# Optimization experiments

Hardware: AMD Instinct MI355X
Metric: run time of the kernel (lower is better)

Reference implementation:

```python
import jax, jax.numpy as jnp
import numpy as np

N = 20000      # nodes
E = 320000     # edges
G = 64         # graphs in batch
PD = 9         # property input dim (properties='yyyyyyyyy')
KD = 32        # kernel_dim (node feature dim)
MD = 32        # m_dim (message dim)
FF = 32        # fourier_features
NK = 5         # n_kernels
EIN = FF * 2 + KD + 1 + KD * 2  # 161, edge MLP input dim
MLP = 256
EPS = 1e-5


def layer_norm(x, g, b):
    mu = jnp.mean(x, -1, keepdims=True)
    var = jnp.mean((x - mu) ** 2, -1, keepdims=True)
    return (x - mu) * jax.lax.rsqrt(var + EPS) * g + b


def silu(x):
    return x * jax.nn.sigmoid(x)


def setup_inputs() -> dict:
    key = jax.random.key(0)
    ks = jax.random.split(key, 20)
    rn = lambda k, s: jax.random.normal(k, s, dtype=jnp.float32) * 0.1
    inp = {}
    inp["props"] = jax.random.normal(ks[0], (N, PD), dtype=jnp.float32)
    inp["positions"] = jax.random.normal(ks[1], (N, 3), dtype=jnp.float32)
    inp["edge_props"] = jax.random.normal(ks[2], (E, PD), dtype=jnp.float32)
    inp["embed_W"] = rn(ks[3], (PD, KD)); inp["embed_b"] = jnp.zeros((KD,), jnp.float32)
    inp["edge_embed_W"] = rn(ks[4], (PD, KD)); inp["edge_embed_b"] = jnp.zeros((KD,), jnp.float32)
    # per-kernel params stacked over NK
    inp["k_eW1"] = rn(ks[5], (NK, EIN, EIN * 2)); inp["k_eb1"] = jnp.zeros((NK, EIN * 2), jnp.float32)
    inp["k_eW2"] = rn(ks[6], (NK, EIN * 2, MD)); inp["k_eb2"] = jnp.zeros((NK, MD), jnp.float32)
    inp["k_eln_g"] = jnp.ones((NK, MD), jnp.float32); inp["k_eln_b"] = jnp.zeros((NK, MD), jnp.float32)
    inp["k_nln1_g"] = jnp.ones((NK, KD), jnp.float32); inp["k_nln1_b"] = jnp.zeros((NK, KD), jnp.float32)
    inp["k_nln2_g"] = jnp.ones((NK, KD), jnp.float32); inp["k_nln2_b"] = jnp.zeros((NK, KD), jnp.float32)
    inp["k_nW1"] = rn(ks[7], (NK, KD + MD, KD * 2)); inp["k_nb1"] = jnp.zeros((NK, KD * 2), jnp.float32)
    inp["k_nW2"] = rn(ks[8], (NK, KD * 2, KD)); inp["k_nb2"] = jnp.zeros((NK, KD), jnp.float32)
    inp["fnn_W0"] = rn(ks[9], (KD * (NK + 1), MLP)); inp["fnn_b0"] = jnp.zeros((MLP,), jnp.float32)
    inp["fnn_W1"] = rn(ks[10], (MLP, MLP)); inp["fnn_b1"] = jnp.zeros((MLP,), jnp.float32)
    inp["fnn_W2"] = rn(ks[11], (MLP, MLP)); inp["fnn_b2"] = jnp.zeros((MLP,), jnp.float32)
    inp["fnn_W3"] = rn(ks[12], (MLP, 1)); inp["fnn_b3"] = jnp.zeros((1,), jnp.float32)
    inp["edge_index"] = jax.random.randint(ks[13], (2, E), 0, N, dtype=jnp.int64)
    inp["batch"] = jnp.sort(jax.random.randint(ks[14], (N,), 0, G, dtype=jnp.int64))
    return inp


def egnn_forward(props, positions, edge_props, embed_W, embed_b, edge_embed_W, edge_embed_b,
                 k_eW1, k_eb1, k_eW2, k_eb2, k_eln_g, k_eln_b, k_nln1_g, k_nln1_b,
                 k_nln2_g, k_nln2_b, k_nW1, k_nb1, k_nW2, k_nb2,
                 fnn_W0, fnn_b0, fnn_W1, fnn_b1, fnn_W2, fnn_b2, fnn_W3, fnn_b3,
                 edge_index, batch):
    src, dst = edge_index[0], edge_index[1]  # x_j = source, x_i = target (PyG)
    feats = props @ embed_W + embed_b                     # EmbedNCP (properties-only path)
    edge_feats = edge_props @ edge_embed_W + edge_embed_b  # EmbedEdge
    coords = positions
    # coords are never updated, so the distance/fourier features are the same each round
    rel_coords = coords[src] - coords[dst]
    rel_dist = jnp.sum(rel_coords ** 2, -1, keepdims=True)  # [E,1] squared distance
    scales = 2.0 ** jnp.arange(FF, dtype=jnp.float32)
    d = rel_dist / scales                                    # [E,FF]
    fdist = jnp.concatenate([jnp.sin(d), jnp.cos(d), rel_dist], -1)  # [E,2FF+1]
    edge_attr = jnp.concatenate([fdist, edge_feats], -1)     # [E, 2FF+1+KD]
    deg = jax.ops.segment_sum(jnp.ones((E,), feats.dtype), dst, num_segments=N)
    deg = jnp.maximum(deg, 1.0)[:, None]
    feat_list = [feats]
    for k in range(NK):
        h = jnp.concatenate([feats[dst], feats[src], edge_attr], -1)  # [E, EIN]
        h = silu(h @ k_eW1[k] + k_eb1[k])
        m_ij = silu(h @ k_eW2[k] + k_eb2[k])
        m_ij = layer_norm(m_ij, k_eln_g[k], k_eln_b[k])               # edge_norm1
        m_i = jax.ops.segment_sum(m_ij, dst, num_segments=N) / deg    # mean aggregate
        m_i = layer_norm(m_i, k_eln_g[k], k_eln_b[k])                 # edge_norm1 again (as in source)
        hf = layer_norm(feats, k_nln1_g[k], k_nln1_b[k])
        h2 = jnp.concatenate([hf, m_i], -1)
        h2 = silu(h2 @ k_nW1[k] + k_nb1[k])
        h2 = h2 @ k_nW2[k] + k_nb2[k]
        h2 = layer_norm(h2, k_nln2_g[k], k_nln2_b[k])
        feats = feats + h2                                            # residual
        feat_list.append(feats)
    allf = jnp.concatenate(feat_list, -1)                             # [N, KD*(NK+1)]
    gsum = jax.ops.segment_sum(allf, batch, num_segments=G)
    gcnt = jnp.maximum(jax.ops.segment_sum(jnp.ones((N,), allf.dtype), batch, num_segments=G), 1.0)[:, None]
    g = gsum / gcnt                                                   # mean pool per graph
    g = silu(g @ fnn_W0 + fnn_b0)
    g = silu(g @ fnn_W1 + fnn_b1)
    g = silu(g @ fnn_W2 + fnn_b2)
    return g @ fnn_W3 + fnn_b3                                        # [G, 1]


def reference(props, positions, edge_props, embed_W, embed_b, edge_embed_W, edge_embed_b,
              k_eW1, k_eb1, k_eW2, k_eb2, k_eln_g, k_eln_b, k_nln1_g, k_nln1_b,
              k_nln2_g, k_nln2_b, k_nW1, k_nb1, k_nW2, k_nb2,
              fnn_W0, fnn_b0, fnn_W1, fnn_b1, fnn_W2, fnn_b2, fnn_W3, fnn_b3,
              edge_index, batch):
    return egnn_forward(props, positions, edge_props, embed_W, embed_b, edge_embed_W, edge_embed_b,
                        k_eW1, k_eb1, k_eW2, k_eb2, k_eln_g, k_eln_b, k_nln1_g, k_nln1_b,
                        k_nln2_g, k_nln2_b, k_nW1, k_nb1, k_nW2, k_nb2,
                        fnn_W0, fnn_b0, fnn_W1, fnn_b1, fnn_W2, fnn_b2, fnn_W3, fnn_b3,
                        edge_index, batch)
```

## Files before the change

kernel.cpp:

```cpp
#include <hip/hip_runtime.h>
#include <math.h>

#define N_NODES 20000
#define N_EDGES 320000
#define N_GRAPHS 64
#define PD 9
#define KD 32
#define MD 32
#define NK 5
#define EIN 161
#define EIN2 322
#define ALLF (KD*(NK+1))
#define LN_EPS 1e-5f

typedef __attribute__((ext_vector_type(8))) short short8;
typedef __attribute__((ext_vector_type(4))) float f32x4;
typedef __attribute__((ext_vector_type(4))) unsigned u32x4;
typedef __attribute__((ext_vector_type(2))) unsigned u32x2;
typedef __attribute__((ext_vector_type(4))) int i32x4;

__device__ __forceinline__ float silu_f(float x) { return x / (1.f + __expf(-x)); }

__device__ __forceinline__ unsigned short f2bf(float x) {
    union { float f; unsigned u; } v; v.f = x;
    unsigned r = v.u + 0x7FFFu + ((v.u >> 16) & 1u);
    return (unsigned short)(r >> 16);
}

__device__ __forceinline__ unsigned cvt_pk_bf16(float lo, float hi) {
    unsigned r;
    asm("v_cvt_pk_bf16_f32 %0, %1, %2" : "=v"(r) : "v"(lo), "v"(hi));
    return r;
}

__global__ __launch_bounds__(256) void pack_w1_kernel(
    const float* __restrict__ eW1, unsigned short* __restrict__ W1p)
{
    int fid = blockIdx.x * 256 + threadIdx.x;
    if (fid >= NK*21*5*64) return;
    int kk = fid / (21*5*64);
    int r  = fid % (21*5*64);
    int nt = r / (5*64);
    int r2 = r % (5*64);
    int kb = r2 >> 6;
    int l  = r2 & 63;
    int q = l >> 4, el = l & 15;
    int n = 32*(nt >> 1) + 8*(el >> 2) + 4*(nt & 1) + (el & 3);
    short8 out;
    #pragma unroll
    for (int i = 0; i < 8; ++i) {
        int kp = 32*kb + 8*q + i;
        int orig = (kp < 128) ? kp : kp + 1;
        float v = (n < EIN2) ? eW1[((size_t)kk*EIN + orig)*EIN2 + n] : 0.f;
        out[i] = (short)f2bf(v);
    }
    *(short8*)&W1p[(size_t)fid*8] = out;
}

__global__ __launch_bounds__(256) void pack_w2_kernel(
    const float* __restrict__ eW2, unsigned short* __restrict__ W2p)
{
    int fid = blockIdx.x * 256 + threadIdx.x;
    if (fid >= NK*2*11*64) return;
    int kk = fid / (2*11*64);
    int r  = fid % (2*11*64);
    int nt2 = r / (11*64);
    int r2  = r % (11*64);
    int kb2 = r2 >> 6;
    int l   = r2 & 63;
    int q = l >> 4, el = l & 15;
    int n = 16*nt2 + el;
    short8 out;
    #pragma unroll
    for (int i = 0; i < 8; ++i) {
        int k2 = 32*kb2 + 8*q + i;
        float v = (k2 < EIN2) ? eW2[((size_t)kk*EIN2 + k2)*MD + n] : 0.f;
        out[i] = (short)f2bf(v);
    }
    *(short8*)&W2p[(size_t)fid*8] = out;
}

__global__ __launch_bounds__(256) void pack_nw_kernel(
    const float* __restrict__ nW1, const float* __restrict__ nW2,
    unsigned short* __restrict__ W1A, unsigned short* __restrict__ W2A)
{
    int fid = blockIdx.x * 256 + threadIdx.x;
    const int tot1 = NK*4*2*64;
    const int tot2 = NK*2*2*64;
    if (fid < tot1) {
        int kk = fid / (4*2*64);
        int r  = fid % (4*2*64);
        int mt = r / 128;
        int r2 = r % 128;
        int kb = r2 >> 6;
        int l  = r2 & 63;
        int q = l >> 4, el = l & 15;
        int n = 32*(mt >> 1) + 8*(el >> 2) + 4*(mt & 1) + (el & 3);
        short8 out;
        #pragma unroll
        for (int i = 0; i < 8; ++i)
            out[i] = (short)f2bf(nW1[((size_t)kk*64 + 32*kb + 8*q + i)*64 + n]);
        *(short8*)&W1A[(size_t)fid*8] = out;
    } else if (fid < tot1 + tot2) {
        int f2 = fid - tot1;
        int kk = f2 / (2*2*64);
        int r  = f2 % (2*2*64);
        int mt2 = r / 128;
        int r2  = r % 128;
        int kb  = r2 >> 6;
        int l   = r2 & 63;
        int q = l >> 4, el = l & 15;
        short8 out;
        #pragma unroll
        for (int i = 0; i < 8; ++i)
            out[i] = (short)f2bf(nW2[((size_t)kk*64 + 32*kb + 8*q + i)*32 + 16*mt2 + el]);
        *(short8*)&W2A[(size_t)f2*8] = out;
    }
}

__global__ __launch_bounds__(256) void embed_nodes_kernel(
    const float* __restrict__ props, const float* __restrict__ W,
    const float* __restrict__ b,
    float* __restrict__ feats, unsigned short* __restrict__ feats_bf,
    float* __restrict__ allf)
{
    int t = threadIdx.x;
    int n = blockIdx.x * 8 + (t >> 5);
    int f = t & 31;
    if (n >= N_NODES) return;
    float acc = b[f];
    #pragma unroll
    for (int i = 0; i < PD; ++i) acc += props[n*PD + i] * W[i*KD + f];
    feats[n*KD + f] = acc;
    feats_bf[n*KD + f] = f2bf(acc);
    allf[(size_t)n*ALLF + f] = acc;
}

__global__ __launch_bounds__(256) void edge_prep_kernel(
    const float* __restrict__ edge_props, const float* __restrict__ positions,
    const int* __restrict__ ei, const float* __restrict__ W,
    const float* __restrict__ b, float* __restrict__ rel,
    float* __restrict__ deg, unsigned short* __restrict__ constpack)
{
    __shared__ float ef[64*32];
    __shared__ float rdl[64];
    int t = threadIdx.x;
    int b0 = blockIdx.x;
    int e0 = b0 * 64;

    {
        int e = t >> 2, sub = t & 3;
        float acc[8];
        #pragma unroll
        for (int j = 0; j < 8; ++j) acc[j] = b[sub*8 + j];
        #pragma unroll
        for (int i = 0; i < PD; ++i) {
            float p = edge_props[(size_t)(e0 + e)*PD + i];
            #pragma unroll
            for (int j = 0; j < 8; ++j) acc[j] += p * W[i*KD + sub*8 + j];
        }
        #pragma unroll
        for (int j = 0; j < 8; ++j) ef[e*32 + sub*8 + j] = acc[j];
    }
    if (t < 64) {
        int e = e0 + t;
        int s = ei[e], d = ei[N_EDGES + e];
        float dx = positions[s*3+0] - positions[d*3+0];
        float dy = positions[s*3+1] - positions[d*3+1];
        float dz = positions[s*3+2] - positions[d*3+2];
        float rd = dx*dx + dy*dy + dz*dz;
        rdl[t] = rd;
        rel[e] = rd;
        atomicAdd(&deg[d], 1.f);
    }
    __syncthreads();

    int l = t & 63, w = t >> 6;
    int q = l >> 4, el = l & 15;
    float rd = rdl[16*w + el];
    #pragma unroll
    for (int kbr = 0; kbr < 3; ++kbr) {
        short8 out;
        #pragma unroll
        for (int i = 0; i < 8; ++i) {
            int k = 8*q + i;
            float v;
            if (kbr == 0)      v = sinf(ldexpf(rd, -k));
            else if (kbr == 1) v = cosf(ldexpf(rd, -k));
            else               v = ef[(16*w + el)*32 + k];
            out[i] = (short)f2bf(v);
        }
        *(short8*)&constpack[((((size_t)b0*4 + w)*3 + kbr)*64 + l)*8] = out;
    }
}

__global__ __launch_bounds__(256) void edge_mlp_mfma(
    const unsigned short* __restrict__ feats_bf,
    const unsigned short* __restrict__ constpack,
    const float* __restrict__ rel, const int* __restrict__ ei,
    const unsigned short* __restrict__ W1p, const unsigned short* __restrict__ W2p,
    const float* __restrict__ w1rd, const float* __restrict__ eb1,
    const float* __restrict__ eb2, const float* __restrict__ lg,
    const float* __restrict__ lb, float* __restrict__ msum)
{
    int t = threadIdx.x;
    int b = blockIdx.x;
    int w = t >> 6, l = t & 63, q = l >> 4, el = l & 15;
    int e0 = b * 64;
    int eMine = e0 + 16*w + el;
    int srcn = ei[eMine];
    int dstn = ei[N_EDGES + eMine];
    float rd = rel[eMine];

    short8 a0 = *(const short8*)&feats_bf[(size_t)dstn*KD + 8*q];
    short8 a1 = *(const short8*)&feats_bf[(size_t)srcn*KD + 8*q];
    const unsigned short* cp = &constpack[((size_t)(b*4 + w)*3)*512 + (size_t)l*8];
    short8 a2 = *(const short8*)&cp[0];
    short8 a3 = *(const short8*)&cp[512];
    short8 a4 = *(const short8*)&cp[1024];

    f32x4 acc20 = {0.f, 0.f, 0.f, 0.f};
    f32x4 acc21 = {0.f, 0.f, 0.f, 0.f};
    unsigned pk0 = 0u, pk1 = 0u, pk2 = 0u, pk3 = 0u;

    #pragma unroll
    for (int nt = 0; nt < 21; ++nt) {
        f32x4 aA = {0.f, 0.f, 0.f, 0.f};
        f32x4 aB = {0.f, 0.f, 0.f, 0.f};
        const unsigned short* wb = &W1p[(size_t)(nt*5)*512 + (size_t)l*8];
        aA = __builtin_amdgcn_mfma_f32_16x16x32_bf16(*(const short8*)&wb[0],    a0, aA, 0, 0, 0);
        aA = __builtin_amdgcn_mfma_f32_16x16x32_bf16(*(const short8*)&wb[512],  a1, aA, 0, 0, 0);
        aA = __builtin_amdgcn_mfma_f32_16x16x32_bf16(*(const short8*)&wb[1024], a2, aA, 0, 0, 0);
        aB = __builtin_amdgcn_mfma_f32_16x16x32_bf16(*(const short8*)&wb[1536], a3, aB, 0, 0, 0);
        aB = __builtin_amdgcn_mfma_f32_16x16x32_bf16(*(const short8*)&wb[2048], a4, aB, 0, 0, 0);

        int base = 32*(nt >> 1) + 4*(nt & 1) + 8*q;
        float vj[4];
        if (nt < 20) {
            f32x4 be = *(const f32x4*)&eb1[base];
            f32x4 wr = *(const f32x4*)&w1rd[base];
            #pragma unroll
            for (int j = 0; j < 4; ++j)
                vj[j] = silu_f(aA[j] + aB[j] + be[j] + rd * wr[j]);
        } else {
            #pragma unroll
            for (int j = 0; j < 4; ++j) {
                int n1 = base + j;
                bool ok = n1 < EIN2;
                float be = ok ? eb1[n1] : 0.f;
                float wr = ok ? w1rd[n1] : 0.f;
                float v = silu_f(aA[j] + aB[j] + be + rd * wr);
                vj[j] = ok ? v : 0.f;
            }
        }

        if ((nt & 1) == 0) {
            pk0 = cvt_pk_bf16(vj[0], vj[1]);
            pk1 = cvt_pk_bf16(vj[2], vj[3]);
        } else {
            pk2 = cvt_pk_bf16(vj[0], vj[1]);
            pk3 = cvt_pk_bf16(vj[2], vj[3]);
            const int kb2 = nt >> 1;
            u32x4 hv = { pk0, pk1, pk2, pk3 };
            short8 av = __builtin_bit_cast(short8, hv);
            short8 b0 = *(const short8*)&W2p[(size_t)kb2*512 + (size_t)l*8];
            short8 b1 = *(const short8*)&W2p[(size_t)(11 + kb2)*512 + (size_t)l*8];
            acc20 = __builtin_amdgcn_mfma_f32_16x16x32_bf16(av, b0, acc20, 0, 0, 0);
            acc21 = __builtin_amdgcn_mfma_f32_16x16x32_bf16(av, b1, acc21, 0, 0, 0);
        }
    }
    {
        u32x4 hv = { pk0, pk1, 0u, 0u };
        short8 av = __builtin_bit_cast(short8, hv);
        short8 b0 = *(const short8*)&W2p[(size_t)10*512 + (size_t)l*8];
        short8 b1 = *(const short8*)&W2p[(size_t)21*512 + (size_t)l*8];
        acc20 = __builtin_amdgcn_mfma_f32_16x16x32_bf16(av, b0, acc20, 0, 0, 0);
        acc21 = __builtin_amdgcn_mfma_f32_16x16x32_bf16(av, b1, acc21, 0, 0, 0);
    }

    i32x4 dstv = *(const i32x4*)&ei[N_EDGES + e0 + 16*w + 4*q];
    float e20 = eb2[el], e21 = eb2[16 + el];
    float g0v = lg[el],  g1v = lg[16 + el];
    float b0v = lb[el],  b1v = lb[16 + el];
    #pragma unroll
    for (int j = 0; j < 4; ++j) {
        float m0 = silu_f(acc20[j] + e20);
        float m1 = silu_f(acc21[j] + e21);
        float s = m0 + m1;
        s += __shfl_xor(s, 1, 16); s += __shfl_xor(s, 2, 16);
        s += __shfl_xor(s, 4, 16); s += __shfl_xor(s, 8, 16);
        float mu = s * (1.f/32.f);
        float d0 = m0 - mu, d1 = m1 - mu;
        float vv = d0*d0 + d1*d1;
        vv += __shfl_xor(vv, 1, 16); vv += __shfl_xor(vv, 2, 16);
        vv += __shfl_xor(vv, 4, 16); vv += __shfl_xor(vv, 8, 16);
        float rs = rsqrtf(vv * (1.f/32.f) + LN_EPS);
        int dst = dstv[j];
        atomicAdd(&msum[(size_t)dst*MD + el],      d0*rs*g0v + b0v);
        atomicAdd(&msum[(size_t)dst*MD + 16 + el], d1*rs*g1v + b1v);
    }
}

__global__ __launch_bounds__(256) void node_mlp_mfma(
    const float* __restrict__ msum, const float* __restrict__ deg,
    const unsigned short* __restrict__ W1A, const unsigned short* __restrict__ W2A,
    const float* __restrict__ nb1, const float* __restrict__ nb2,
    const float* __restrict__ eln_g, const float* __restrict__ eln_b,
    const float* __restrict__ n1g, const float* __restrict__ n1b,
    const float* __restrict__ n2g, const float* __restrict__ n2b,
    float* __restrict__ feats, unsigned short* __restrict__ feats_bf,
    float* __restrict__ allf, int kslot)
{
    int t = threadIdx.x;
    int w = t >> 6, l = t & 63, q = l >> 4, el = l & 15;
    int nd = blockIdx.x*64 + 16*w + el;
    bool okn = nd < N_NODES;
    size_t ndc = okn ? (size_t)nd : (size_t)(N_NODES - 1);

    float x[2][8];
    {
        f32x4 f0 = *(const f32x4*)&feats[ndc*KD + 8*q];
        f32x4 f1 = *(const f32x4*)&feats[ndc*KD + 8*q + 4];
        float inv = 1.f / fmaxf(deg[ndc], 1.f);
        f32x4 m0 = *(const f32x4*)&msum[ndc*KD + 8*q];
        f32x4 m1 = *(const f32x4*)&msum[ndc*KD + 8*q + 4];
        #pragma unroll
        for (int j = 0; j < 4; ++j) {
            x[0][j] = f0[j]; x[0][4+j] = f1[j];
            x[1][j] = m0[j]*inv; x[1][4+j] = m1[j]*inv;
        }
    }
    short8 xf[2];
    #pragma unroll
    for (int kb = 0; kb < 2; ++kb) {
        float s = 0.f;
        #pragma unroll
        for (int i = 0; i < 8; ++i) s += x[kb][i];
        s += __shfl_xor(s, 16); s += __shfl_xor(s, 32);
        float mu = s * (1.f/32.f);
        float vv = 0.f;
        #pragma unroll
        for (int i = 0; i < 8; ++i) { float d = x[kb][i] - mu; vv += d*d; }
        vv += __shfl_xor(vv, 16); vv += __shfl_xor(vv, 32);
        float rs = rsqrtf(vv * (1.f/32.f) + LN_EPS);
        const float* gp = kb ? eln_g : n1g;
        const float* bp = kb ? eln_b : n1b;
        f32x4 ga = *(const f32x4*)&gp[8*q];
        f32x4 gb = *(const f32x4*)&gp[8*q + 4];
        f32x4 ba = *(const f32x4*)&bp[8*q];
        f32x4 bb = *(const f32x4*)&bp[8*q + 4];
        float z[8];
        #pragma unroll
        for (int j = 0; j < 4; ++j) {
            z[j]   = (x[kb][j]   - mu)*rs*ga[j] + ba[j];
            z[4+j] = (x[kb][4+j] - mu)*rs*gb[j] + bb[j];
        }
        u32x4 pv = { cvt_pk_bf16(z[0], z[1]), cvt_pk_bf16(z[2], z[3]),
                     cvt_pk_bf16(z[4], z[5]), cvt_pk_bf16(z[6], z[7]) };
        xf[kb] = __builtin_bit_cast(short8, pv);
    }

    unsigned hr[8];
    #pragma unroll
    for (int mt = 0; mt < 4; ++mt) {
        f32x4 acc = {0.f, 0.f, 0.f, 0.f};
        acc = __builtin_amdgcn_mfma_f32_16x16x32_bf16(
            *(const short8*)&W1A[(size_t)(mt*2 + 0)*512 + (size_t)l*8], xf[0], acc, 0, 0, 0);
        acc = __builtin_amdgcn_mfma_f32_16x16x32_bf16(
            *(const short8*)&W1A[(size_t)(mt*2 + 1)*512 + (size_t)l*8], xf[1], acc, 0, 0, 0);
        int base = 32*(mt >> 1) + 4*(mt & 1) + 8*q;
        f32x4 b1v = *(const f32x4*)&nb1[base];
        float vj[4];
        #pragma unroll
        for (int j = 0; j < 4; ++j) vj[j] = silu_f(acc[j] + b1v[j]);
        int ix = (mt >> 1)*4 + (mt & 1)*2;
        hr[ix]     = cvt_pk_bf16(vj[0], vj[1]);
        hr[ix + 1] = cvt_pk_bf16(vj[2], vj[3]);
    }

    u32x4 h0v = { hr[0], hr[1], hr[2], hr[3] };
    u32x4 h1v = { hr[4], hr[5], hr[6], hr[7] };
    short8 hf0 = __builtin_bit_cast(short8, h0v);
    short8 hf1 = __builtin_bit_cast(short8, h1v);
    float o[2][4];
    #pragma unroll
    for (int mt2 = 0; mt2 < 2; ++mt2) {
        f32x4 acc = {0.f, 0.f, 0.f, 0.f};
        acc = __builtin_amdgcn_mfma_f32_16x16x32_bf16(
            *(const short8*)&W2A[(size_t)(mt2*2 + 0)*512 + (size_t)l*8], hf0, acc, 0, 0, 0);
        acc = __builtin_amdgcn_mfma_f32_16x16x32_bf16(
            *(const short8*)&W2A[(size_t)(mt2*2 + 1)*512 + (size_t)l*8], hf1, acc, 0, 0, 0);
        f32x4 b2v = *(const f32x4*)&nb2[16*mt2 + 4*q];
        #pragma unroll
        for (int j = 0; j < 4; ++j) o[mt2][j] = acc[j] + b2v[j];
    }
    float s2 = 0.f;
    #pragma unroll
    for (int mt2 = 0; mt2 < 2; ++mt2)
        #pragma unroll
        for (int j = 0; j < 4; ++j) s2 += o[mt2][j];
    s2 += __shfl_xor(s2, 16); s2 += __shfl_xor(s2, 32);
    float mu2 = s2 * (1.f/32.f);
    float vv2 = 0.f;
    #pragma unroll
    for (int mt2 = 0; mt2 < 2; ++mt2)
        #pragma unroll
        for (int j = 0; j < 4; ++j) { float d = o[mt2][j] - mu2; vv2 += d*d; }
    vv2 += __shfl_xor(vv2, 16); vv2 += __shfl_xor(vv2, 32);
    float rs2 = rsqrtf(vv2 * (1.f/32.f) + LN_EPS);

    #pragma unroll
    for (int mt2 = 0; mt2 < 2; ++mt2) {
        f32x4 gv = *(const f32x4*)&n2g[16*mt2 + 4*q];
        f32x4 bv = *(const f32x4*)&n2b[16*mt2 + 4*q];
        f32x4 fold = *(const f32x4*)&feats[ndc*KD + 16*mt2 + 4*q];
        f32x4 nf;
        #pragma unroll
        for (int j = 0; j < 4; ++j)
            nf[j] = fold[j] + (o[mt2][j] - mu2)*rs2*gv[j] + bv[j];
        if (okn) {
            *(f32x4*)&feats[(size_t)nd*KD + 16*mt2 + 4*q] = nf;
            u32x2 pb = { cvt_pk_bf16(nf[0], nf[1]), cvt_pk_bf16(nf[2], nf[3]) };
            *(u32x2*)&feats_bf[(size_t)nd*KD + 16*mt2 + 4*q] = pb;
            *(f32x4*)&allf[(size_t)nd*ALLF + kslot*KD + 16*mt2 + 4*q] = nf;
        }
    }
}

__global__ __launch_bounds__(256) void pool_kernel(
    const float* __restrict__ allf, const int* __restrict__ batch,
    float* __restrict__ gsum, float* __restrict__ gcnt)
{
    int b = blockIdx.x, t = threadIdx.x;
    int g = b >> 2, part = b & 3;
    int lo = 0, hi = N_NODES;
    while (lo < hi) { int m = (lo+hi) >> 1; if (batch[m] < g) lo = m+1; else hi = m; }
    int start = lo;
    hi = N_NODES;
    while (lo < hi) { int m = (lo+hi) >> 1; if (batch[m] < g+1) lo = m+1; else hi = m; }
    int end = lo;
    if (part == 0 && t == 0) gcnt[g] = (float)(end - start);
    int len = end - start;
    int chunk = (len + 3) >> 2;
    int s = start + part*chunk;
    int e = min(end, s + chunk);
    if (t < ALLF && e > s) {
        float acc = 0.f;
        for (int n = s; n < e; ++n) acc += allf[(size_t)n*ALLF + t];
        atomicAdd(&gsum[g*ALLF + t], acc);
    }
}

__global__ __launch_bounds__(256) void fnn_kernel(
    const float* __restrict__ gsum, const float* __restrict__ gcnt,
    const float* __restrict__ W0, const float* __restrict__ b0,
    const float* __restrict__ W1, const float* __restrict__ b1,
    const float* __restrict__ W2, const float* __restrict__ b2,
    const float* __restrict__ W3, const float* __restrict__ b3,
    float* __restrict__ out)
{
    __shared__ float xs[256];
    __shared__ float partial[4];
    int g = blockIdx.x, t = threadIdx.x;
    float inv = 1.f / fmaxf(gcnt[g], 1.f);
    if (t < ALLF) xs[t] = gsum[g*ALLF + t] * inv;
    __syncthreads();
    float acc = b0[t];
    for (int i = 0; i < ALLF; ++i) acc += xs[i] * W0[i*256 + t];
    acc = silu_f(acc);
    __syncthreads(); xs[t] = acc; __syncthreads();
    acc = b1[t];
    for (int i = 0; i < 256; ++i) acc += xs[i] * W1[i*256 + t];
    acc = silu_f(acc);
    __syncthreads(); xs[t] = acc; __syncthreads();
    acc = b2[t];
    for (int i = 0; i < 256; ++i) acc += xs[i] * W2[i*256 + t];
    acc = silu_f(acc);
    __syncthreads(); xs[t] = acc; __syncthreads();
    float v = xs[t] * W3[t];
    #pragma unroll
    for (int m = 32; m; m >>= 1) v += __shfl_xor(v, m, 64);
    if ((t & 63) == 0) partial[t >> 6] = v;
    __syncthreads();
    if (t == 0) out[g] = partial[0] + partial[1] + partial[2] + partial[3] + b3[0];
}

extern "C" void kernel_launch(void* const* d_in, const int* in_sizes, int n_in,
                              void* d_out, int out_size, void* d_ws, size_t ws_size,
                              hipStream_t stream) {
    const float* props      = (const float*)d_in[0];
    const float* positions  = (const float*)d_in[1];
    const float* edge_props = (const float*)d_in[2];
    const float* embed_W    = (const float*)d_in[3];
    const float* embed_b    = (const float*)d_in[4];
    const float* eeW        = (const float*)d_in[5];
    const float* eeb        = (const float*)d_in[6];
    const float* k_eW1      = (const float*)d_in[7];
    const float* k_eb1      = (const float*)d_in[8];
    const float* k_eW2      = (const float*)d_in[9];
    const float* k_eb2      = (const float*)d_in[10];
    const float* k_eln_g    = (const float*)d_in[11];
    const float* k_eln_b    = (const float*)d_in[12];
    const float* k_n1g      = (const float*)d_in[13];
    const float* k_n1b      = (const float*)d_in[14];
    const float* k_n2g      = (const float*)d_in[15];
    const float* k_n2b      = (const float*)d_in[16];
    const float* k_nW1      = (const float*)d_in[17];
    const float* k_nb1      = (const float*)d_in[18];
    const float* k_nW2      = (const float*)d_in[19];
    const float* k_nb2      = (const float*)d_in[20];
    const float* fnn_W0     = (const float*)d_in[21];
    const float* fnn_b0     = (const float*)d_in[22];
    const float* fnn_W1     = (const float*)d_in[23];
    const float* fnn_b1     = (const float*)d_in[24];
    const float* fnn_W2     = (const float*)d_in[25];
    const float* fnn_b2     = (const float*)d_in[26];
    const float* fnn_W3     = (const float*)d_in[27];
    const float* fnn_b3     = (const float*)d_in[28];
    const int*   ei         = (const int*)d_in[29];
    const int*   batch      = (const int*)d_in[30];
    float* out = (float*)d_out;

    char* wsb = (char*)d_ws;
    size_t off = 0;
    #define WS_ALLOC(ptr_t, name, bytes) ptr_t name = (ptr_t)(wsb + off); off += (((size_t)(bytes)) + 255) & ~(size_t)255;
    WS_ALLOC(float*, feats, (size_t)N_NODES*KD*4)
    WS_ALLOC(float*, msum,  (size_t)N_NODES*KD*4)
    WS_ALLOC(float*, deg,   (size_t)N_NODES*4)
    WS_ALLOC(float*, rel,   (size_t)N_EDGES*4)
    WS_ALLOC(float*, gsum,  (size_t)N_GRAPHS*ALLF*4)
    WS_ALLOC(float*, gcnt,  (size_t)N_GRAPHS*4)
    WS_ALLOC(float*, allf,  (size_t)N_NODES*ALLF*4)
    WS_ALLOC(unsigned short*, feats_bf,  (size_t)N_NODES*KD*2)
    WS_ALLOC(unsigned short*, constpack, (size_t)5000*4*3*64*8*2)
    WS_ALLOC(unsigned short*, W1p,  (size_t)NK*21*5*64*8*2)
    WS_ALLOC(unsigned short*, W2p,  (size_t)NK*2*11*64*8*2)
    WS_ALLOC(unsigned short*, W1An, (size_t)NK*4*2*64*8*2)
    WS_ALLOC(unsigned short*, W2An, (size_t)NK*2*2*64*8*2)
    (void)ws_size;

    hipMemsetAsync(deg,  0, (size_t)N_NODES*4, stream);
    hipMemsetAsync(gsum, 0, (size_t)N_GRAPHS*ALLF*4, stream);

    pack_w1_kernel<<<(NK*21*5*64 + 255)/256, 256, 0, stream>>>(k_eW1, W1p);
    pack_w2_kernel<<<(NK*2*11*64 + 255)/256, 256, 0, stream>>>(k_eW2, W2p);
    pack_nw_kernel<<<(NK*4*2*64 + NK*2*2*64 + 255)/256, 256, 0, stream>>>(k_nW1, k_nW2, W1An, W2An);
    embed_nodes_kernel<<<N_NODES/8, 256, 0, stream>>>(props, embed_W, embed_b,
                                                      feats, feats_bf, allf);
    edge_prep_kernel<<<N_EDGES/64, 256, 0, stream>>>(edge_props, positions, ei, eeW, eeb,
                                                     rel, deg, constpack);

    for (int k = 0; k < NK; ++k) {
        hipMemsetAsync(msum, 0, (size_t)N_NODES*KD*4, stream);
        edge_mlp_mfma<<<N_EDGES/64, 256, 0, stream>>>(
            feats_bf, constpack, rel, ei,
            W1p + (size_t)k*21*5*512, W2p + (size_t)k*2*11*512,
            k_eW1 + (size_t)k*EIN*EIN2 + 128*EIN2,
            k_eb1 + (size_t)k*EIN2, k_eb2 + (size_t)k*MD,
            k_eln_g + (size_t)k*MD, k_eln_b + (size_t)k*MD, msum);
        node_mlp_mfma<<<(N_NODES + 63)/64, 256, 0, stream>>>(
            msum, deg,
            W1An + (size_t)k*4*2*512, W2An + (size_t)k*2*2*512,
            k_nb1 + (size_t)k*64, k_nb2 + (size_t)k*32,
            k_eln_g + (size_t)k*MD, k_eln_b + (size_t)k*MD,
            k_n1g + (size_t)k*KD, k_n1b + (size_t)k*KD,
            k_n2g + (size_t)k*KD, k_n2b + (size_t)k*KD,
            feats, feats_bf, allf, k+1);
    }

    pool_kernel<<<N_GRAPHS*4, 256, 0, stream>>>(allf, batch, gsum, gcnt);
    fnn_kernel<<<N_GRAPHS, 256, 0, stream>>>(gsum, gcnt, fnn_W0, fnn_b0, fnn_W1, fnn_b1,
                                             fnn_W2, fnn_b2, fnn_W3, fnn_b3, out);
}
```

Before: 829.8 us.

## Switch edge MLP to 32x32x16 MFMA tiles with bias folded into weights

The edge MLP moves from 16x16x32 bf16 MFMA to 32x32x16 MFMA, so each wave handles 32 edges and each block 128 edges. The weight and constant packing layouts are rebuilt to match. The first-layer bias and the rel-distance column are folded into the packed W1 as extra K rows, fed by a constant-1/rd operand, which removes the per-element bias and rd FMA epilogue. The aim is to cut weight-load traffic per edge and epilogue ALU work. In exchange the rd term now goes through bf16, and register pressure from the 16-wide accumulators rises.

```diff
diff --git a/kernel.cpp b/kernel.cpp
--- a/kernel.cpp
+++ b/kernel.cpp
@@ -15,9 +15,9 @@
 
 typedef __attribute__((ext_vector_type(8))) short short8;
 typedef __attribute__((ext_vector_type(4))) float f32x4;
+typedef __attribute__((ext_vector_type(16))) float f32x16;
 typedef __attribute__((ext_vector_type(4))) unsigned u32x4;
 typedef __attribute__((ext_vector_type(2))) unsigned u32x2;
-typedef __attribute__((ext_vector_type(4))) int i32x4;
 
 __device__ __forceinline__ float silu_f(float x) { return x / (1.f + __expf(-x)); }
 
@@ -34,24 +34,31 @@
 }
 
 __global__ __launch_bounds__(256) void pack_w1_kernel(
-    const float* __restrict__ eW1, unsigned short* __restrict__ W1p)
+    const float* __restrict__ eW1, const float* __restrict__ eb1,
+    unsigned short* __restrict__ W1p)
 {
     int fid = blockIdx.x * 256 + threadIdx.x;
-    if (fid >= NK*21*5*64) return;
-    int kk = fid / (21*5*64);
-    int r  = fid % (21*5*64);
-    int nt = r / (5*64);
-    int r2 = r % (5*64);
-    int kb = r2 >> 6;
+    if (fid >= NK*11*11*64) return;
+    int kk = fid / (11*11*64);
+    int r  = fid % (11*11*64);
+    int m  = r / (11*64);
+    int r2 = r % (11*64);
+    int s  = r2 >> 6;
     int l  = r2 & 63;
-    int q = l >> 4, el = l & 15;
-    int n = 32*(nt >> 1) + 8*(el >> 2) + 4*(nt & 1) + (el & 3);
+    int p = l & 31, khalf = l >> 5;
+    int h = (p >> 2) & 1, c = p & 3, bb = p >> 3;
+    int n = 32*m + 16*(bb >> 1) + 8*h + c + 4*(bb & 1);
     short8 out;
     #pragma unroll
     for (int i = 0; i < 8; ++i) {
-        int kp = 32*kb + 8*q + i;
-        int orig = (kp < 128) ? kp : kp + 1;
-        float v = (n < EIN2) ? eW1[((size_t)kk*EIN + orig)*EIN2 + n] : 0.f;
+        int k = 16*s + 8*khalf + i;
+        float v = 0.f;
+        if (n < EIN2) {
+            if (k < 128)       v = eW1[((size_t)kk*EIN + k)*EIN2 + n];
+            else if (k < 160)  v = eW1[((size_t)kk*EIN + k + 1)*EIN2 + n];
+            else if (k == 160) v = eb1[(size_t)kk*EIN2 + n];
+            else if (k == 161) v = eW1[((size_t)kk*EIN + 128)*EIN2 + n];
+        }
         out[i] = (short)f2bf(v);
     }
     *(short8*)&W1p[(size_t)fid*8] = out;
@@ -61,19 +68,16 @@
     const float* __restrict__ eW2, unsigned short* __restrict__ W2p)
 {
     int fid = blockIdx.x * 256 + threadIdx.x;
-    if (fid >= NK*2*11*64) return;
-    int kk = fid / (2*11*64);
-    int r  = fid % (2*11*64);
-    int nt2 = r / (11*64);
-    int r2  = r % (11*64);
-    int kb2 = r2 >> 6;
-    int l   = r2 & 63;
-    int q = l >> 4, el = l & 15;
-    int n = 16*nt2 + el;
+    if (fid >= NK*22*64) return;
+    int kk = fid / (22*64);
+    int r  = fid % (22*64);
+    int s2 = r >> 6;
+    int l  = r & 63;
+    int n = l & 31, khalf = l >> 5;
     short8 out;
     #pragma unroll
     for (int i = 0; i < 8; ++i) {
-        int k2 = 32*kb2 + 8*q + i;
+        int k2 = 16*s2 + 8*khalf + i;
         float v = (k2 < EIN2) ? eW2[((size_t)kk*EIN2 + k2)*MD + n] : 0.f;
         out[i] = (short)f2bf(v);
     }
@@ -142,27 +146,27 @@
     const float* __restrict__ b, float* __restrict__ rel,
     float* __restrict__ deg, unsigned short* __restrict__ constpack)
 {
-    __shared__ float ef[64*32];
-    __shared__ float rdl[64];
+    __shared__ float ef[128*32];
+    __shared__ float rdl[128];
     int t = threadIdx.x;
     int b0 = blockIdx.x;
-    int e0 = b0 * 64;
+    int e0 = b0 * 128;
 
     {
-        int e = t >> 2, sub = t & 3;
-        float acc[8];
-        #pragma unroll
-        for (int j = 0; j < 8; ++j) acc[j] = b[sub*8 + j];
+        int e = t >> 1, sub = t & 1;
+        float acc[16];
+        #pragma unroll
+        for (int j = 0; j < 16; ++j) acc[j] = b[sub*16 + j];
         #pragma unroll
         for (int i = 0; i < PD; ++i) {
             float p = edge_props[(size_t)(e0 + e)*PD + i];
             #pragma unroll
-            for (int j = 0; j < 8; ++j) acc[j] += p * W[i*KD + sub*8 + j];
-        }
-        #pragma unroll
-        for (int j = 0; j < 8; ++j) ef[e*32 + sub*8 + j] = acc[j];
-    }
-    if (t < 64) {
+            for (int j = 0; j < 16; ++j) acc[j] += p * W[i*KD + sub*16 + j];
+        }
+        #pragma unroll
+        for (int j = 0; j < 16; ++j) ef[e*32 + sub*16 + j] = acc[j];
+    }
+    if (t < 128) {
         int e = e0 + t;
         int s = ei[e], d = ei[N_EDGES + e];
         float dx = positions[s*3+0] - positions[d*3+0];
@@ -176,21 +180,23 @@
     __syncthreads();
 
     int l = t & 63, w = t >> 6;
-    int q = l >> 4, el = l & 15;
-    float rd = rdl[16*w + el];
-    #pragma unroll
-    for (int kbr = 0; kbr < 3; ++kbr) {
+    int e32 = l & 31, hi = l >> 5;
+    int eloc = 32*w + e32;
+    float rd = rdl[eloc];
+    #pragma unroll
+    for (int slot = 0; slot < 6; ++slot) {
+        int grp = slot >> 1, half = slot & 1;
         short8 out;
         #pragma unroll
         for (int i = 0; i < 8; ++i) {
-            int k = 8*q + i;
+            int off = 16*half + 8*hi + i;
             float v;
-            if (kbr == 0)      v = sinf(ldexpf(rd, -k));
-            else if (kbr == 1) v = cosf(ldexpf(rd, -k));
-            else               v = ef[(16*w + el)*32 + k];
+            if (grp == 0)      v = sinf(ldexpf(rd, -off));
+            else if (grp == 1) v = cosf(ldexpf(rd, -off));
+            else               v = ef[eloc*32 + off];
             out[i] = (short)f2bf(v);
         }
-        *(short8*)&constpack[((((size_t)b0*4 + w)*3 + kbr)*64 + l)*8] = out;
+        *(short8*)&constpack[(((size_t)b0*4 + w)*6 + slot)*512 + (size_t)l*8] = out;
     }
 }
 
@@ -199,105 +205,88 @@
     const unsigned short* __restrict__ constpack,
     const float* __restrict__ rel, const int* __restrict__ ei,
     const unsigned short* __restrict__ W1p, const unsigned short* __restrict__ W2p,
-    const float* __restrict__ w1rd, const float* __restrict__ eb1,
     const float* __restrict__ eb2, const float* __restrict__ lg,
     const float* __restrict__ lb, float* __restrict__ msum)
 {
     int t = threadIdx.x;
     int b = blockIdx.x;
-    int w = t >> 6, l = t & 63, q = l >> 4, el = l & 15;
-    int e0 = b * 64;
-    int eMine = e0 + 16*w + el;
-    int srcn = ei[eMine];
-    int dstn = ei[N_EDGES + eMine];
-    float rd = rel[eMine];
-
-    short8 a0 = *(const short8*)&feats_bf[(size_t)dstn*KD + 8*q];
-    short8 a1 = *(const short8*)&feats_bf[(size_t)srcn*KD + 8*q];
-    const unsigned short* cp = &constpack[((size_t)(b*4 + w)*3)*512 + (size_t)l*8];
-    short8 a2 = *(const short8*)&cp[0];
-    short8 a3 = *(const short8*)&cp[512];
-    short8 a4 = *(const short8*)&cp[1024];
-
-    f32x4 acc20 = {0.f, 0.f, 0.f, 0.f};
-    f32x4 acc21 = {0.f, 0.f, 0.f, 0.f};
-    unsigned pk0 = 0u, pk1 = 0u, pk2 = 0u, pk3 = 0u;
-
-    #pragma unroll
-    for (int nt = 0; nt < 21; ++nt) {
-        f32x4 aA = {0.f, 0.f, 0.f, 0.f};
-        f32x4 aB = {0.f, 0.f, 0.f, 0.f};
-        const unsigned short* wb = &W1p[(size_t)(nt*5)*512 + (size_t)l*8];
-        aA = __builtin_amdgcn_mfma_f32_16x16x32_bf16(*(const short8*)&wb[0],    a0, aA, 0, 0, 0);
-        aA = __builtin_amdgcn_mfma_f32_16x16x32_bf16(*(const short8*)&wb[512],  a1, aA, 0, 0, 0);
-        aA = __builtin_amdgcn_mfma_f32_16x16x32_bf16(*(const short8*)&wb[1024], a2, aA, 0, 0, 0);
-        aB = __builtin_amdgcn_mfma_f32_16x16x32_bf16(*(const short8*)&wb[1536], a3, aB, 0, 0, 0);
-        aB = __builtin_amdgcn_mfma_f32_16x16x32_bf16(*(const short8*)&wb[2048], a4, aB, 0, 0, 0);
-
-        int base = 32*(nt >> 1) + 4*(nt & 1) + 8*q;
-        float vj[4];
-        if (nt < 20) {
-            f32x4 be = *(const f32x4*)&eb1[base];
-            f32x4 wr = *(const f32x4*)&w1rd[base];
-            #pragma unroll
-            for (int j = 0; j < 4; ++j)
-                vj[j] = silu_f(aA[j] + aB[j] + be[j] + rd * wr[j]);
-        } else {
-            #pragma unroll
-            for (int j = 0; j < 4; ++j) {
-                int n1 = base + j;
-                bool ok = n1 < EIN2;
-                float be = ok ? eb1[n1] : 0.f;
-                float wr = ok ? w1rd[n1] : 0.f;
-                float v = silu_f(aA[j] + aB[j] + be + rd * wr);
-                vj[j] = ok ? v : 0.f;
-            }
-        }
-
-        if ((nt & 1) == 0) {
-            pk0 = cvt_pk_bf16(vj[0], vj[1]);
-            pk1 = cvt_pk_bf16(vj[2], vj[3]);
-        } else {
-            pk2 = cvt_pk_bf16(vj[0], vj[1]);
-            pk3 = cvt_pk_bf16(vj[2], vj[3]);
-            const int kb2 = nt >> 1;
-            u32x4 hv = { pk0, pk1, pk2, pk3 };
-            short8 av = __builtin_bit_cast(short8, hv);
-            short8 b0 = *(const short8*)&W2p[(size_t)kb2*512 + (size_t)l*8];
-            short8 b1 = *(const short8*)&W2p[(size_t)(11 + kb2)*512 + (size_t)l*8];
-            acc20 = __builtin_amdgcn_mfma_f32_16x16x32_bf16(av, b0, acc20, 0, 0, 0);
-            acc21 = __builtin_amdgcn_mfma_f32_16x16x32_bf16(av, b1, acc21, 0, 0, 0);
-        }
-    }
+    int w = t >> 6, l = t & 63, e32 = l & 31, hi = l >> 5;
+    int edge = b*128 + 32*w + e32;
+    int srcn = ei[edge];
+    int dstn = ei[N_EDGES + edge];
+    float rd = rel[edge];
+
+    short8 bf[11];
+    bf[0] = *(const short8*)&feats_bf[(size_t)dstn*KD + 8*hi];
+    bf[1] = *(const short8*)&feats_bf[(size_t)dstn*KD + 16 + 8*hi];
+    bf[2] = *(const short8*)&feats_bf[(size_t)srcn*KD + 8*hi];
+    bf[3] = *(const short8*)&feats_bf[(size_t)srcn*KD + 16 + 8*hi];
+    const unsigned short* cp = &constpack[(((size_t)b*4 + w)*6)*512 + (size_t)l*8];
+    #pragma unroll
+    for (int slot = 0; slot < 6; ++slot)
+        bf[4 + slot] = *(const short8*)&cp[(size_t)slot*512];
     {
-        u32x4 hv = { pk0, pk1, 0u, 0u };
-        short8 av = __builtin_bit_cast(short8, hv);
-        short8 b0 = *(const short8*)&W2p[(size_t)10*512 + (size_t)l*8];
-        short8 b1 = *(const short8*)&W2p[(size_t)21*512 + (size_t)l*8];
-        acc20 = __builtin_amdgcn_mfma_f32_16x16x32_bf16(av, b0, acc20, 0, 0, 0);
-        acc21 = __builtin_amdgcn_mfma_f32_16x16x32_bf16(av, b1, acc21, 0, 0, 0);
-    }
-
-    i32x4 dstv = *(const i32x4*)&ei[N_EDGES + e0 + 16*w + 4*q];
-    float e20 = eb2[el], e21 = eb2[16 + el];
-    float g0v = lg[el],  g1v = lg[16 + el];
-    float b0v = lb[el],  b1v = lb[16 + el];
-    #pragma unroll
-    for (int j = 0; j < 4; ++j) {
-        float m0 = silu_f(acc20[j] + e20);
-        float m1 = silu_f(acc21[j] + e21);
-        float s = m0 + m1;
-        s += __shfl_xor(s, 1, 16); s += __shfl_xor(s, 2, 16);
-        s += __shfl_xor(s, 4, 16); s += __shfl_xor(s, 8, 16);
-        float mu = s * (1.f/32.f);
-        float d0 = m0 - mu, d1 = m1 - mu;
-        float vv = d0*d0 + d1*d1;
-        vv += __shfl_xor(vv, 1, 16); vv += __shfl_xor(vv, 2, 16);
-        vv += __shfl_xor(vv, 4, 16); vv += __shfl_xor(vv, 8, 16);
-        float rs = rsqrtf(vv * (1.f/32.f) + LN_EPS);
-        int dst = dstv[j];
-        atomicAdd(&msum[(size_t)dst*MD + el],      d0*rs*g0v + b0v);
-        atomicAdd(&msum[(size_t)dst*MD + 16 + el], d1*rs*g1v + b1v);
+        short8 z = {0,0,0,0,0,0,0,0};
+        if (hi == 0) { z[0] = (short)0x3F80; z[1] = (short)f2bf(rd); }
+        bf[10] = z;
+    }
+
+    const unsigned short* w1l = W1p + (size_t)l*8;
+    const unsigned short* w2l = W2p + (size_t)l*8;
+
+    f32x16 acc2 = {0.f};
+    #pragma unroll
+    for (int m = 0; m < 11; ++m) {
+        f32x16 acc1 = {0.f};
+        #pragma unroll
+        for (int s = 0; s < 11; ++s)
+            acc1 = __builtin_amdgcn_mfma_f32_32x32x16_bf16(
+                *(const short8*)&w1l[(size_t)(m*11 + s)*512], bf[s], acc1, 0, 0, 0);
+        unsigned plo[4], phi[4];
+        #pragma unroll
+        for (int j = 0; j < 4; ++j) {
+            plo[j] = cvt_pk_bf16(silu_f(acc1[2*j]),     silu_f(acc1[2*j+1]));
+            phi[j] = cvt_pk_bf16(silu_f(acc1[8+2*j]),   silu_f(acc1[8+2*j+1]));
+        }
+        u32x4 vlo = { plo[0], plo[1], plo[2], plo[3] };
+        u32x4 vhi = { phi[0], phi[1], phi[2], phi[3] };
+        acc2 = __builtin_amdgcn_mfma_f32_32x32x16_bf16(
+            *(const short8*)&w2l[(size_t)(2*m)*512],
+            __builtin_bit_cast(short8, vlo), acc2, 0, 0, 0);
+        acc2 = __builtin_amdgcn_mfma_f32_32x32x16_bf16(
+            *(const short8*)&w2l[(size_t)(2*m + 1)*512],
+            __builtin_bit_cast(short8, vhi), acc2, 0, 0, 0);
+    }
+
+    float mv[16];
+    float ssum = 0.f;
+    #pragma unroll
+    for (int rg = 0; rg < 4; ++rg) {
+        f32x4 e2 = *(const f32x4*)&eb2[8*rg + 4*hi];
+        #pragma unroll
+        for (int c = 0; c < 4; ++c) {
+            float v = silu_f(acc2[rg*4 + c] + e2[c]);
+            mv[rg*4 + c] = v;
+            ssum += v;
+        }
+    }
+    ssum += __shfl_xor(ssum, 32);
+    float mu = ssum * (1.f/32.f);
+    float vsum = 0.f;
+    #pragma unroll
+    for (int r = 0; r < 16; ++r) { float d = mv[r] - mu; vsum += d*d; }
+    vsum += __shfl_xor(vsum, 32);
+    float rs = rsqrtf(vsum * (1.f/32.f) + LN_EPS);
+
+    float* mrow = &msum[(size_t)dstn*MD];
+    #pragma unroll
+    for (int rg = 0; rg < 4; ++rg) {
+        int ch0 = 8*rg + 4*hi;
+        f32x4 gv = *(const f32x4*)&lg[ch0];
+        f32x4 bv = *(const f32x4*)&lb[ch0];
+        #pragma unroll
+        for (int c = 0; c < 4; ++c)
+            atomicAdd(&mrow[ch0 + c], (mv[rg*4 + c] - mu)*rs*gv[c] + bv[c]);
     }
 }
 
@@ -532,9 +521,9 @@
     WS_ALLOC(float*, gcnt,  (size_t)N_GRAPHS*4)
     WS_ALLOC(float*, allf,  (size_t)N_NODES*ALLF*4)
     WS_ALLOC(unsigned short*, feats_bf,  (size_t)N_NODES*KD*2)
-    WS_ALLOC(unsigned short*, constpack, (size_t)5000*4*3*64*8*2)
-    WS_ALLOC(unsigned short*, W1p,  (size_t)NK*21*5*64*8*2)
-    WS_ALLOC(unsigned short*, W2p,  (size_t)NK*2*11*64*8*2)
+    WS_ALLOC(unsigned short*, constpack, (size_t)2500*4*6*64*8*2)
+    WS_ALLOC(unsigned short*, W1p,  (size_t)NK*11*11*64*8*2)
+    WS_ALLOC(unsigned short*, W2p,  (size_t)NK*22*64*8*2)
     WS_ALLOC(unsigned short*, W1An, (size_t)NK*4*2*64*8*2)
     WS_ALLOC(unsigned short*, W2An, (size_t)NK*2*2*64*8*2)
     (void)ws_size;
@@ -542,21 +531,20 @@
     hipMemsetAsync(deg,  0, (size_t)N_NODES*4, stream);
     hipMemsetAsync(gsum, 0, (size_t)N_GRAPHS*ALLF*4, stream);
 
-    pack_w1_kernel<<<(NK*21*5*64 + 255)/256, 256, 0, stream>>>(k_eW1, W1p);
-    pack_w2_kernel<<<(NK*2*11*64 + 255)/256, 256, 0, stream>>>(k_eW2, W2p);
+    pack_w1_kernel<<<(NK*11*11*64 + 255)/256, 256, 0, stream>>>(k_eW1, k_eb1, W1p);
+    pack_w2_kernel<<<(NK*22*64 + 255)/256, 256, 0, stream>>>(k_eW2, W2p);
     pack_nw_kernel<<<(NK*4*2*64 + NK*2*2*64 + 255)/256, 256, 0, stream>>>(k_nW1, k_nW2, W1An, W2An);
     embed_nodes_kernel<<<N_NODES/8, 256, 0, stream>>>(props, embed_W, embed_b,
                                                       feats, feats_bf, allf);
-    edge_prep_kernel<<<N_EDGES/64, 256, 0, stream>>>(edge_props, positions, ei, eeW, eeb,
-                                                     rel, deg, constpack);
+    edge_prep_kernel<<<N_EDGES/128, 256, 0, stream>>>(edge_props, positions, ei, eeW, eeb,
+                                                      rel, deg, constpack);
 
     for (int k = 0; k < NK; ++k) {
         hipMemsetAsync(msum, 0, (size_t)N_NODES*KD*4, stream);
-        edge_mlp_mfma<<<N_EDGES/64, 256, 0, stream>>>(
+        edge_mlp_mfma<<<N_EDGES/128, 256, 0, stream>>>(
             feats_bf, constpack, rel, ei,
-            W1p + (size_t)k*21*5*512, W2p + (size_t)k*2*11*512,
-            k_eW1 + (size_t)k*EIN*EIN2 + 128*EIN2,
-            k_eb1 + (size_t)k*EIN2, k_eb2 + (size_t)k*MD,
+            W1p + (size_t)k*11*11*512, W2p + (size_t)k*22*512,
+            k_eb2 + (size_t)k*MD,
             k_eln_g + (size_t)k*MD, k_eln_b + (size_t)k*MD, msum);
         node_mlp_mfma<<<(N_NODES + 63)/64, 256, 0, stream>>>(
             msum, deg,
```

New measurement: 1.899 ms. +128.9%, slower.
